# Kernel optimization log

Hardware: AMD Instinct MI355X
Metric: run time of the kernel (lower is better)

The kernel has to match this reference:

```python
import jax, jax.numpy as jnp
import numpy as np
import math

B_, L_, D_, N_ = 8, 2048, 1024, 64


def _ln(x, g, b):
    m = jnp.mean(x, axis=-1, keepdims=True)
    v = jnp.mean((x - m) ** 2, axis=-1, keepdims=True)
    return (x - m) / jnp.sqrt(v + 1e-5) * g + b


def _ssm_kernel(A, Bp, Cp, Dp, L):
    # diagonal SSM: lambda = exp(diag(A)); k[l] = C diag(lambda)^l B + D  -> shape (L,)
    a = jnp.diagonal(A)                                   # (N,)
    powers = jnp.exp(jnp.arange(L)[:, None] * a[None, :])  # (L, N) = lambda^l
    return powers @ (Bp[:, 0] * Cp[0]) + Dp[0]             # (L,)


def _causal_conv(h, k):
    # y[:, t, :] = sum_{j<=t} k[j] * h[:, t-j, :]  via zero-padded FFT (same math, O(L log L))
    L = h.shape[1]
    n = 2 * L
    Hf = jnp.fft.rfft(h, n=n, axis=1)
    Kf = jnp.fft.rfft(k, n=n)
    return jnp.fft.irfft(Hf * Kf[None, :, None], n=n, axis=1)[:, :L]


def _timestep_embedding(t, dim):
    half = dim // 2
    freqs = jnp.exp(jnp.arange(half) * (-math.log(10000.0) / (half - 1)))
    ang = t[:, None] * freqs[None, :]
    return jnp.concatenate([jnp.sin(ang), jnp.cos(ang)], axis=1)  # (B, dim)


def _conv1d(x, w, b):
    # x: (B, C, L), w: (O, I, 3) torch layout, padding=1
    y = jax.lax.conv_general_dilated(x, w, (1,), [(1, 1)],
                                     dimension_numbers=('NCH', 'OIH', 'NCH'))
    return y + b[None, :, None]


def setup_inputs():
    key = jax.random.key(0)
    ks = jax.random.split(key, 26)
    d = {}
    d['x'] = jax.random.normal(ks[0], (B_, L_, D_), jnp.float32)
    d['t'] = jax.random.uniform(ks[1], (B_,), jnp.float32) * 1000.0
    d['beta1'] = jax.random.uniform(ks[2], (1,), jnp.float32)
    d['beta2'] = jax.random.uniform(ks[3], (1,), jnp.float32)
    sc = 1.0 / math.sqrt(D_)
    d['Wi'] = jax.random.normal(ks[4], (D_, D_), jnp.float32) * sc
    d['bi'] = jnp.zeros((D_,), jnp.float32)
    d['Wo'] = jax.random.normal(ks[5], (D_, D_), jnp.float32) * sc
    d['bo'] = jnp.zeros((D_,), jnp.float32)
    d['w1'] = jax.random.normal(ks[6], (D_, D_, 3), jnp.float32) * 0.02
    d['bc1'] = jnp.zeros((D_,), jnp.float32)
    d['w2'] = jax.random.normal(ks[7], (D_, D_, 3), jnp.float32) * 0.02
    d['bc2'] = jnp.zeros((D_,), jnp.float32)
    d['g1'] = jnp.ones((D_,), jnp.float32)
    d['b1'] = jnp.zeros((D_,), jnp.float32)
    d['g2'] = jnp.ones((D_,), jnp.float32)
    d['b2'] = jnp.zeros((D_,), jnp.float32)
    # SSM params (std 0.001 on A keeps exp(l*a) bounded for l up to L)
    d['Af'] = jax.random.normal(ks[8], (N_, N_), jnp.float32) * 0.001
    d['Bf'] = jax.random.normal(ks[9], (N_, 1), jnp.float32) * 0.01
    d['Cf'] = jax.random.normal(ks[10], (1, N_), jnp.float32) * 0.01
    d['Df'] = jax.random.normal(ks[11], (1,), jnp.float32) * 0.01
    d['Ab'] = jax.random.normal(ks[12], (N_, N_), jnp.float32) * 0.001
    d['Bb'] = jax.random.normal(ks[13], (N_, 1), jnp.float32) * 0.01
    d['Cb'] = jax.random.normal(ks[14], (1, N_), jnp.float32) * 0.01
    d['Db'] = jax.random.normal(ks[15], (1,), jnp.float32) * 0.01
    return d


def reference(x, t, beta1, beta2, Wi, bi, Wo, bo, w1, bc1, w2, bc2,
              g1, b1, g2, b2, Af, Bf, Cf, Df, Ab, Bb, Cb, Db):
    Bsz, L, D = x.shape
    h = x @ Wi + bi
    h = _ln(h, g1, b1)
    # local conv branch
    hT = jnp.transpose(h, (0, 2, 1))                 # (B, D, L)
    co = jax.nn.silu(_conv1d(hT, w1, bc1))
    co = _conv1d(co, w2, bc2)
    conv_out = jnp.transpose(co, (0, 2, 1))          # (B, L, D)
    # bidirectional SSM global convolutions
    kf = _ssm_kernel(Af, Bf, Cf, Df, L)
    h_fwd = _causal_conv(h, kf)
    kb = _ssm_kernel(Ab, Bb, Cb, Db, L)
    h_bwd = jnp.flip(_causal_conv(jnp.flip(h, axis=1), kb), axis=1)
    # timestep-conditioned mixing
    noise_scale = jax.nn.sigmoid(_timestep_embedding(t, D))[:, None, :]  # (B,1,D)
    h = h_fwd * (beta1[0] * noise_scale) + h_bwd * (beta2[0] * noise_scale) + conv_out
    h = h @ Wo + bo
    h = _ln(h, g2, b2)
    return x + h
```

## Files before the change

kernel.cpp:

```cpp
#include <hip/hip_runtime.h>

#define Bq 8
#define Lq 2048
#define Dq 1024
#define LPq 2050

typedef unsigned short u16;
typedef __attribute__((ext_vector_type(8))) short bf16x8;
typedef __attribute__((ext_vector_type(4))) float f32x4;

__device__ __forceinline__ u16 f2bf(float f) {
  unsigned u = __float_as_uint(f);
  u += 0x7FFFu + ((u >> 16) & 1u);
  return (u16)(u >> 16);
}
__device__ __forceinline__ float bf2f(u16 s) {
  return __uint_as_float(((unsigned)s) << 16);
}
__device__ __forceinline__ void gld16(const u16* g, u16* l) {
  __builtin_amdgcn_global_load_lds((const __attribute__((address_space(1))) void*)g,
                                   (__attribute__((address_space(3))) void*)l, 16, 0, 0);
}


__global__ __launch_bounds__(256) void prep_small(
    const float* __restrict__ t, const float* __restrict__ beta1, const float* __restrict__ beta2,
    const float* __restrict__ Af, const float* __restrict__ Bf, const float* __restrict__ Cf, const float* __restrict__ Df,
    const float* __restrict__ Ab, const float* __restrict__ Bb, const float* __restrict__ Cb, const float* __restrict__ Db,
    float* __restrict__ kf, float* __restrict__ kb,
    float* __restrict__ c1, float* __restrict__ c2,
    u16* __restrict__ hpad, u16* __restrict__ copad) {
  int tid = blockIdx.x * 256 + threadIdx.x;
  if (blockIdx.x < 8) {
    int l = tid;
    float sf = Df[0], sb = Db[0];
    for (int n = 0; n < 64; n++) {
      sf += __expf((float)l * Af[n * 64 + n]) * (Bf[n] * Cf[n]);
      sb += __expf((float)l * Ab[n * 64 + n]) * (Bb[n] * Cb[n]);
    }
    kf[l] = sf; kb[l] = sb;
  } else if (blockIdx.x < 40) {
    int i = tid - 2048;
    int b = i >> 10, d = i & 1023;
    float tb = t[b];
    float e;
    if (d < 512) {
      float f = __expf((float)d * (-logf(10000.f) / 511.f));
      e = sinf(tb * f);
    } else {
      float f = __expf((float)(d - 512) * (-logf(10000.f) / 511.f));
      e = cosf(tb * f);
    }
    float ns = 1.f / (1.f + __expf(-e));
    c1[i] = beta1[0] * ns;
    c2[i] = beta2[0] * ns;
  } else {
    int i = tid - 10240;
    if (i < 32768) {
      int d = i & 1023;
      int j = i >> 10;
      int arr = j & 1, r = (j >> 1) & 1, b = j >> 2;
      size_t off = (size_t)b * LPq * Dq + (r ? (size_t)(LPq - 1) * Dq : 0) + d;
      if (arr == 0) hpad[off] = 0;
      else          copad[off] = 0;
    }
  }
}

__global__ __launch_bounds__(256) void cast_x(const float* __restrict__ x, u16* __restrict__ xb) {
  size_t i = ((size_t)blockIdx.x * 256 + threadIdx.x) * 8;
  float4 a = *(const float4*)(x + i);
  float4 b = *(const float4*)(x + i + 4);
  u16 o[8] = {f2bf(a.x), f2bf(a.y), f2bf(a.z), f2bf(a.w),
              f2bf(b.x), f2bf(b.y), f2bf(b.z), f2bf(b.w)};
  *(bf16x8*)(xb + i) = *(const bf16x8*)o;
}

__global__ __launch_bounds__(256) void trans_w(const float* __restrict__ W, u16* __restrict__ Wt) {
  __shared__ float tile[64][65];
  int bx = blockIdx.x & 15, by = blockIdx.x >> 4;
  int tx = threadIdx.x & 63, tw = threadIdx.x >> 6;
  for (int r = tw; r < 64; r += 4)
    tile[r][tx] = W[(size_t)(by * 64 + r) * 1024 + bx * 64 + tx];
  __syncthreads();
  for (int r = tw; r < 64; r += 4)
    Wt[(size_t)(bx * 64 + r) * 1024 + by * 64 + tx] = f2bf(tile[tx][r]);
}

__global__ __launch_bounds__(256) void trans_w3(const float* __restrict__ w, u16* __restrict__ Wt) {
  int idx = blockIdx.x * 256 + threadIdx.x;
  int o = idx / 3072, rem = idx % 3072;
  int dt = rem >> 10, i = rem & 1023;
  Wt[idx] = f2bf(w[(size_t)o * 3072 + i * 3 + dt]);
}

__global__ __launch_bounds__(256) void tf_fill(const float* __restrict__ kf, const float* __restrict__ kb,
                                               u16* __restrict__ Tf, u16* __restrict__ Tb) {
  int idx = blockIdx.x * 256 + threadIdx.x;
  int tr = idx >> 9, j0 = (idx & 511) * 4;
  ushort4 vf, vb;
  int j;
  j = j0 + 0; vf.x = (tr >= j) ? f2bf(kf[tr - j]) : (u16)0; vb.x = (j >= tr) ? f2bf(kb[j - tr]) : (u16)0;
  j = j0 + 1; vf.y = (tr >= j) ? f2bf(kf[tr - j]) : (u16)0; vb.y = (j >= tr) ? f2bf(kb[j - tr]) : (u16)0;
  j = j0 + 2; vf.z = (tr >= j) ? f2bf(kf[tr - j]) : (u16)0; vb.z = (j >= tr) ? f2bf(kb[j - tr]) : (u16)0;
  j = j0 + 3; vf.w = (tr >= j) ? f2bf(kf[tr - j]) : (u16)0; vb.w = (j >= tr) ? f2bf(kb[j - tr]) : (u16)0;
  *(ushort4*)(Tf + (size_t)tr * 2048 + j0) = vf;
  *(ushort4*)(Tb + (size_t)tr * 2048 + j0) = vb;
}

__global__ __launch_bounds__(256) void trans_h(const u16* __restrict__ hpad, u16* __restrict__ ht) {
  __shared__ u16 tile[64][66];
  int b = blockIdx.z;
  int lt = blockIdx.x * 64, dt = blockIdx.y * 64;
  int tx = threadIdx.x & 15, ty = threadIdx.x >> 4;
  const u16* src = hpad + (size_t)b * LPq * Dq + (size_t)(lt + 1 + ty) * Dq + dt + tx * 4;
#pragma unroll
  for (int i = 0; i < 4; i++) {
    int r = ty + i * 16;
    ushort4 v = *(const ushort4*)(src + (size_t)i * 16 * Dq);
    tile[tx * 4 + 0][r] = v.x;
    tile[tx * 4 + 1][r] = v.y;
    tile[tx * 4 + 2][r] = v.z;
    tile[tx * 4 + 3][r] = v.w;
  }
  __syncthreads();
#pragma unroll
  for (int i = 0; i < 4; i++) {
    int d = ty + i * 16;
    ushort4 v;
    v.x = tile[d][tx * 4 + 0];
    v.y = tile[d][tx * 4 + 1];
    v.z = tile[d][tx * 4 + 2];
    v.w = tile[d][tx * 4 + 3];
    *(ushort4*)(ht + ((size_t)b * Dq + dt + d) * Lq + lt + tx * 4) = v;
  }
}


__global__ __launch_bounds__(256) void ln1_k(const u16* __restrict__ h0, u16* __restrict__ hpad,
                                             const float* __restrict__ g, const float* __restrict__ be) {
  int w = threadIdx.x >> 6, lane = threadIdx.x & 63;
  int r = blockIdx.x * 4 + w;
  int d0 = lane * 16;
  const u16* hp = h0 + (size_t)r * 1024 + d0;
  bf16x8 va = *(const bf16x8*)hp;
  bf16x8 vb = *(const bf16x8*)(hp + 8);
  float v[16];
#pragma unroll
  for (int i = 0; i < 8; i++) { v[i] = bf2f((u16)va[i]); v[8 + i] = bf2f((u16)vb[i]); }
  float s = 0.f, q = 0.f;
#pragma unroll
  for (int i = 0; i < 16; i++) { s += v[i]; q += v[i] * v[i]; }
#pragma unroll
  for (int o = 32; o > 0; o >>= 1) { s += __shfl_xor(s, o); q += __shfl_xor(q, o); }
  float mean = s * (1.f / 1024.f);
  float rstd = rsqrtf(q * (1.f / 1024.f) - mean * mean + 1e-5f);
  const float4* g4 = (const float4*)(g + d0);
  const float4* b4 = (const float4*)(be + d0);
  u16 o16[16];
#pragma unroll
  for (int i = 0; i < 4; i++) {
    float4 gv = g4[i], bv = b4[i];
    o16[i * 4 + 0] = f2bf((v[i * 4 + 0] - mean) * rstd * gv.x + bv.x);
    o16[i * 4 + 1] = f2bf((v[i * 4 + 1] - mean) * rstd * gv.y + bv.y);
    o16[i * 4 + 2] = f2bf((v[i * 4 + 2] - mean) * rstd * gv.z + bv.z);
    o16[i * 4 + 3] = f2bf((v[i * 4 + 3] - mean) * rstd * gv.w + bv.w);
  }
  int b_ = r >> 11, l = r & 2047;
  u16* dst = hpad + ((size_t)b_ * LPq + l + 1) * Dq + d0;
  *(bf16x8*)dst = *(const bf16x8*)o16;
  *(bf16x8*)(dst + 8) = *(const bf16x8*)(o16 + 8);
}

__global__ __launch_bounds__(256) void ln2_k(const u16* __restrict__ hp, const float* __restrict__ x,
                                             const float* __restrict__ g, const float* __restrict__ be,
                                             float* __restrict__ out) {
  int w = threadIdx.x >> 6, lane = threadIdx.x & 63;
  size_t r = (size_t)blockIdx.x * 4 + w;
  int d0 = lane * 16;
  size_t base = r * 1024 + d0;
  const u16* h = hp + base;
  bf16x8 va = *(const bf16x8*)h;
  bf16x8 vb = *(const bf16x8*)(h + 8);
  float v[16];
#pragma unroll
  for (int i = 0; i < 8; i++) { v[i] = bf2f((u16)va[i]); v[8 + i] = bf2f((u16)vb[i]); }
  float s = 0.f, q = 0.f;
#pragma unroll
  for (int i = 0; i < 16; i++) { s += v[i]; q += v[i] * v[i]; }
#pragma unroll
  for (int o = 32; o > 0; o >>= 1) { s += __shfl_xor(s, o); q += __shfl_xor(q, o); }
  float mean = s * (1.f / 1024.f);
  float rstd = rsqrtf(q * (1.f / 1024.f) - mean * mean + 1e-5f);
  const float4* g4 = (const float4*)(g + d0);
  const float4* b4 = (const float4*)(be + d0);
  const float4* x4 = (const float4*)(x + base);
  float4* o4 = (float4*)(out + base);
#pragma unroll
  for (int i = 0; i < 4; i++) {
    float4 gv = g4[i], bv = b4[i], xv = x4[i];
    float4 o;
    o.x = xv.x + (v[i * 4 + 0] - mean) * rstd * gv.x + bv.x;
    o.y = xv.y + (v[i * 4 + 1] - mean) * rstd * gv.y + bv.y;
    o.z = xv.z + (v[i * 4 + 2] - mean) * rstd * gv.z + bv.z;
    o.w = xv.w + (v[i * 4 + 3] - mean) * rstd * gv.w + bv.w;
    o4[i] = o;
  }
}

__device__ __forceinline__ void gemm_core(const u16* __restrict__ Ab, int lda,
                                          const u16* __restrict__ Bb, int ldb,
                                          int ks, int NS, u16* lds,
                                          f32x4 (&acc)[8][4]) {
  const int t = threadIdx.x;
  const int lane = t & 63, w = t >> 6;
  const int g = w >> 2, j = w & 3;
  const int p1 = t >> 3;
  const int c1 = (t & 7) ^ (p1 & 7);
  const int row1 = (p1 << 1) | (c1 >> 2), f1 = c1 & 3;
  const int q2 = t + 512;
  const int p2 = q2 >> 3;
  const int c2 = (q2 & 7) ^ (p2 & 7);
  const int row2 = (p2 << 1) | (c2 >> 2), f2 = c2 & 3;
  const int aoff1 = row1 * lda + f1 * 8;
  const int aoff2 = row2 * lda + f2 * 8;
  const int boff1 = row1 * ldb + f1 * 8;
  const int boff2 = row2 * ldb + f2 * 8;
  u16* wA1 = lds + t * 8;
  u16* wA2 = lds + 4096 + t * 8;
  u16* wB1 = lds + 8192 + t * 8;
  u16* wB2 = lds + 12288 + t * 8;
  const int frow = lane & 15, fkc = lane >> 4;
  const int arow = g * 128 + frow;
  const int pa = arow >> 1, ca = ((arow & 1) << 2) | fkc;
  const int abase = pa * 64 + ((ca ^ (pa & 7)) << 3);
  const int brow = j * 64 + frow;
  const int pb = brow >> 1, cb = ((brow & 1) << 2) | fkc;
  const int bbase = 8192 + pb * 64 + ((cb ^ (pb & 7)) << 3);

#define STAGE_A(s_) { int sl_ = ((s_) & 3) * 16384; const u16* g_ = Ab + ks + (s_) * 32; \
    gld16(g_ + aoff1, wA1 + sl_); gld16(g_ + aoff2, wA2 + sl_); }
#define STAGE_B(s_) { int sl_ = ((s_) & 3) * 16384; const u16* g_ = Bb + ks + (s_) * 32; \
    gld16(g_ + boff1, wB1 + sl_); gld16(g_ + boff2, wB2 + sl_); }

  STAGE_A(0); STAGE_B(0);
  STAGE_A(1); STAGE_B(1);
  STAGE_A(2); STAGE_B(2);

  for (int s = 0; s < NS; s++) {
    const u16* sl = lds + (s & 3) * 16384;
    if (s <= NS - 3)      { asm volatile("s_waitcnt vmcnt(8)" ::: "memory"); }
    else if (s == NS - 2) { asm volatile("s_waitcnt vmcnt(4)" ::: "memory"); }
    else                  { asm volatile("s_waitcnt vmcnt(0)" ::: "memory"); }
    asm volatile("s_barrier" ::: "memory");
    if (s + 3 < NS) STAGE_A(s + 3);
    bf16x8 bq[4], af[4];
#pragma unroll
    for (int nf = 0; nf < 4; nf++) bq[nf] = *(const bf16x8*)(sl + bbase + nf * 512);
#pragma unroll
    for (int mf = 0; mf < 4; mf++) af[mf] = *(const bf16x8*)(sl + abase + mf * 512);
    __builtin_amdgcn_s_setprio(1);
#pragma unroll
    for (int mf = 0; mf < 4; mf++)
#pragma unroll
      for (int nf = 0; nf < 4; nf++)
        acc[mf][nf] = __builtin_amdgcn_mfma_f32_16x16x32_bf16(af[mf], bq[nf], acc[mf][nf], 0, 0, 0);
    __builtin_amdgcn_s_setprio(0);
    if (s + 3 < NS) STAGE_B(s + 3);
#pragma unroll
    for (int mf = 0; mf < 4; mf++) af[mf] = *(const bf16x8*)(sl + abase + 2048 + mf * 512);
    __builtin_amdgcn_s_setprio(1);
#pragma unroll
    for (int mf = 0; mf < 4; mf++)
#pragma unroll
      for (int nf = 0; nf < 4; nf++)
        acc[4 + mf][nf] = __builtin_amdgcn_mfma_f32_16x16x32_bf16(af[mf], bq[nf], acc[4 + mf][nf], 0, 0, 0);
    __builtin_amdgcn_s_setprio(0);
  }
#undef STAGE_A
#undef STAGE_B
}

template <int MODE>
__global__ __launch_bounds__(512, 2) void gemm8(
    const u16* __restrict__ A, int lda, long abstr,
    const u16* __restrict__ Bw, int ldb,
    u16* __restrict__ Out, long obstr,
    const u16* __restrict__ aux,
    const float* __restrict__ bias, int K, int nbm) {
  __shared__ __align__(16) u16 lds[65536];
  int mb = blockIdx.x % nbm, nb = blockIdx.x / nbm;
  int m0 = mb * 256, n0 = nb * 256;
  int batch = m0 >> 11, r0 = m0 & 2047;
  const u16* Ab = A + (size_t)batch * abstr + (size_t)r0 * lda;
  const u16* Bb = Bw + (size_t)n0 * ldb;
  f32x4 acc[8][4] = {};
  gemm_core(Ab, lda, Bb, ldb, 0, K >> 5, lds, acc);
  int lane = threadIdx.x & 63, w = threadIdx.x >> 6;
  int g = w >> 2, j = w & 3;
  int frow = lane & 15;
  u16* ob = Out + (size_t)batch * obstr;
  const u16* ab2 = (MODE == 3) ? aux + (size_t)batch * obstr : nullptr;
#pragma unroll
  for (int mf = 0; mf < 8; mf++) {
    int row = r0 + g * 128 + mf * 16 + ((lane >> 4) << 2);
#pragma unroll
    for (int nf = 0; nf < 4; nf++) {
      int col = n0 + j * 64 + nf * 16 + frow;
      float bv = bias[col];
      size_t base = (size_t)row * 1024 + col;
      f32x4 a = acc[mf][nf];
#pragma unroll
      for (int i = 0; i < 4; i++) {
        float v = a[i] + bv;
        if (MODE == 1) v = v / (1.f + __expf(-v));
        if (MODE == 3) v += bf2f(ob[base + (size_t)i * 1024]) + bf2f(ab2[base + (size_t)i * 1024]);
        ob[base + (size_t)i * 1024] = f2bf(v);
      }
    }
  }
}

__global__ __launch_bounds__(512, 2) void ssm8(
    const u16* __restrict__ Tf, const u16* __restrict__ Tb,
    const u16* __restrict__ Ht,
    const float* __restrict__ c1, const float* __restrict__ c2,
    u16* __restrict__ outF, u16* __restrict__ outB) {
  __shared__ __align__(16) u16 lds[65536];
  int id = blockIdx.x;
  int dir = id >> 8, r = id & 255;
  int mb = r & 7, nb = r >> 3;
  int m0 = mb * 256, n0 = nb * 256;
  int ks = dir ? m0 : 0;
  int ke = dir ? 2048 : m0 + 256;
  const u16* Tm = dir ? Tb : Tf;
  const u16* Ab = Tm + (size_t)m0 * 2048;
  const u16* Bb = Ht + (size_t)n0 * 2048;
  f32x4 acc[8][4] = {};
  gemm_core(Ab, 2048, Bb, 2048, ks, (ke - ks) >> 5, lds, acc);
  const float* cs = dir ? c2 : c1;
  u16* out = dir ? outB : outF;
  int lane = threadIdx.x & 63, w = threadIdx.x >> 6;
  int g = w >> 2, j = w & 3;
  int frow = lane & 15;
#pragma unroll
  for (int mf = 0; mf < 8; mf++) {
    int row = m0 + g * 128 + mf * 16 + ((lane >> 4) << 2);
#pragma unroll
    for (int nf = 0; nf < 4; nf++) {
      int col = n0 + j * 64 + nf * 16 + frow;
      int b = col >> 10, d = col & 1023;
      float cv = cs[col];
      u16* op = out + ((size_t)b * Lq + row) * 1024 + d;
      f32x4 a = acc[mf][nf];
#pragma unroll
      for (int i = 0; i < 4; i++)
        op[(size_t)i * 1024] = f2bf(a[i] * cv);
    }
  }
}


extern "C" void kernel_launch(void* const* d_in, const int* in_sizes, int n_in,
                              void* d_out, int out_size, void* d_ws, size_t ws_size,
                              hipStream_t stream) {
  const float* x   = (const float*)d_in[0];
  const float* tt  = (const float*)d_in[1];
  const float* be1 = (const float*)d_in[2];
  const float* be2 = (const float*)d_in[3];
  const float* Wi  = (const float*)d_in[4];
  const float* bi  = (const float*)d_in[5];
  const float* Wo  = (const float*)d_in[6];
  const float* bo  = (const float*)d_in[7];
  const float* w1  = (const float*)d_in[8];
  const float* bc1 = (const float*)d_in[9];
  const float* w2  = (const float*)d_in[10];
  const float* bc2 = (const float*)d_in[11];
  const float* g1  = (const float*)d_in[12];
  const float* b1  = (const float*)d_in[13];
  const float* g2  = (const float*)d_in[14];
  const float* b2  = (const float*)d_in[15];
  const float* Af  = (const float*)d_in[16];
  const float* Bf  = (const float*)d_in[17];
  const float* Cf  = (const float*)d_in[18];
  const float* Df  = (const float*)d_in[19];
  const float* Ab  = (const float*)d_in[20];
  const float* Bb  = (const float*)d_in[21];
  const float* Cb  = (const float*)d_in[22];
  const float* Db  = (const float*)d_in[23];

  char* p = (char*)d_ws;
  constexpr size_t SZ_h0   = (size_t)16384 * 1024 * 2;
  constexpr size_t SZ_hpad = (size_t)Bq * LPq * Dq * 2;
  constexpr size_t SZ_ht   = (size_t)Bq * Dq * Lq * 2;
  constexpr size_t SZ_hmix = (size_t)16384 * 1024 * 2;
  constexpr size_t SZ_T    = (size_t)2048 * 2048 * 2;
  constexpr size_t SZ_wt   = (size_t)1024 * 1024 * 2;
  constexpr size_t SZ_w3t  = (size_t)1024 * 3072 * 2;

  size_t off = 0;
  u16* h0    = (u16*)(p + off); off += SZ_h0;
  u16* hpad  = (u16*)(p + off); off += SZ_hpad;
  u16* ht    = (u16*)(p + off); off += SZ_ht;
  u16* copad = (u16*)(p + off); off += SZ_hpad;
  u16* hmixF = (u16*)(p + off); off += SZ_hmix;
  u16* Tf    = (u16*)(p + off); off += SZ_T;
  u16* Tb    = (u16*)(p + off); off += SZ_T;
  u16* wit   = (u16*)(p + off); off += SZ_wt;
  u16* wot   = (u16*)(p + off); off += SZ_wt;
  u16* w1t   = (u16*)(p + off); off += SZ_w3t;
  u16* w2t   = (u16*)(p + off); off += SZ_w3t;
  float* kf  = (float*)(p + off); off += 8192;
  float* kb  = (float*)(p + off); off += 8192;
  float* c1  = (float*)(p + off); off += 32768;
  float* c2  = (float*)(p + off); off += 32768;
  u16* xb    = hmixF;
  u16* hmixB = h0;

  const long BSTR = (long)2048 * 1024;
  const long PSTR = (long)LPq * 1024;

  prep_small<<<dim3(168), dim3(256), 0, stream>>>(tt, be1, be2, Af, Bf, Cf, Df,
                                                  Ab, Bb, Cb, Db, kf, kb, c1, c2, hpad, copad);
  cast_x<<<dim3(8192), dim3(256), 0, stream>>>(x, xb);
  trans_w<<<dim3(256), dim3(256), 0, stream>>>(Wi, wit);
  trans_w<<<dim3(256), dim3(256), 0, stream>>>(Wo, wot);
  trans_w3<<<dim3(12288), dim3(256), 0, stream>>>(w1, w1t);
  trans_w3<<<dim3(12288), dim3(256), 0, stream>>>(w2, w2t);
  tf_fill<<<dim3(4096), dim3(256), 0, stream>>>(kf, kb, Tf, Tb);

  gemm8<0><<<dim3(256), dim3(512), 0, stream>>>(xb, 1024, BSTR, wit, 1024, h0, BSTR, nullptr, bi, 1024, 64);
  ln1_k<<<dim3(4096), dim3(256), 0, stream>>>(h0, hpad, g1, b1);
  trans_h<<<dim3(32, 16, 8), dim3(256), 0, stream>>>(hpad, ht);
  gemm8<1><<<dim3(256), dim3(512), 0, stream>>>(hpad, 1024, PSTR, w1t, 3072, copad + 1024, PSTR, nullptr, bc1, 3072, 64);
  ssm8<<<dim3(512), dim3(512), 0, stream>>>(Tf, Tb, ht, c1, c2, hmixF, hmixB);
  gemm8<3><<<dim3(256), dim3(512), 0, stream>>>(copad, 1024, PSTR, w2t, 3072, hmixF, BSTR, hmixB, bc2, 3072, 64);
  gemm8<0><<<dim3(256), dim3(512), 0, stream>>>(hmixF, 1024, BSTR, wot, 1024, h0, BSTR, nullptr, bo, 1024, 64);
  ln2_k<<<dim3(4096), dim3(256), 0, stream>>>(h0, x, g2, b2, (float*)d_out);
}
```

Measured before the change: 492.6 us.

## Merge prep kernels and co-schedule conv1 GEMM with SSM GEMMs in one launch

Folds the six weight, input and Toeplitz preparation kernels into a single block-indexed launch, and vectorises the w3 transpose to four elements per thread. The first conv GEMM and the two triangular SSM Toeplitz GEMMs now run as one 768-block launch. The forward-direction SSM tiles are reordered so the longest K ranges start first, which should improve load balance against the conv tiles. This cuts launch overhead and fills the GPU with independent work, but the merged kernels share one register and LDS budget and use a fixed branching layout.

```diff
diff --git a/kernel.cpp b/kernel.cpp
--- a/kernel.cpp
+++ b/kernel.cpp
@@ -67,45 +67,60 @@
   }
 }
 
-__global__ __launch_bounds__(256) void cast_x(const float* __restrict__ x, u16* __restrict__ xb) {
-  size_t i = ((size_t)blockIdx.x * 256 + threadIdx.x) * 8;
-  float4 a = *(const float4*)(x + i);
-  float4 b = *(const float4*)(x + i + 4);
-  u16 o[8] = {f2bf(a.x), f2bf(a.y), f2bf(a.z), f2bf(a.w),
-              f2bf(b.x), f2bf(b.y), f2bf(b.z), f2bf(b.w)};
-  *(bf16x8*)(xb + i) = *(const bf16x8*)o;
-}
-
-__global__ __launch_bounds__(256) void trans_w(const float* __restrict__ W, u16* __restrict__ Wt) {
-  __shared__ float tile[64][65];
-  int bx = blockIdx.x & 15, by = blockIdx.x >> 4;
-  int tx = threadIdx.x & 63, tw = threadIdx.x >> 6;
-  for (int r = tw; r < 64; r += 4)
-    tile[r][tx] = W[(size_t)(by * 64 + r) * 1024 + bx * 64 + tx];
-  __syncthreads();
-  for (int r = tw; r < 64; r += 4)
-    Wt[(size_t)(bx * 64 + r) * 1024 + by * 64 + tx] = f2bf(tile[tx][r]);
-}
-
-__global__ __launch_bounds__(256) void trans_w3(const float* __restrict__ w, u16* __restrict__ Wt) {
-  int idx = blockIdx.x * 256 + threadIdx.x;
-  int o = idx / 3072, rem = idx % 3072;
-  int dt = rem >> 10, i = rem & 1023;
-  Wt[idx] = f2bf(w[(size_t)o * 3072 + i * 3 + dt]);
-}
-
-__global__ __launch_bounds__(256) void tf_fill(const float* __restrict__ kf, const float* __restrict__ kb,
-                                               u16* __restrict__ Tf, u16* __restrict__ Tb) {
-  int idx = blockIdx.x * 256 + threadIdx.x;
-  int tr = idx >> 9, j0 = (idx & 511) * 4;
-  ushort4 vf, vb;
-  int j;
-  j = j0 + 0; vf.x = (tr >= j) ? f2bf(kf[tr - j]) : (u16)0; vb.x = (j >= tr) ? f2bf(kb[j - tr]) : (u16)0;
-  j = j0 + 1; vf.y = (tr >= j) ? f2bf(kf[tr - j]) : (u16)0; vb.y = (j >= tr) ? f2bf(kb[j - tr]) : (u16)0;
-  j = j0 + 2; vf.z = (tr >= j) ? f2bf(kf[tr - j]) : (u16)0; vb.z = (j >= tr) ? f2bf(kb[j - tr]) : (u16)0;
-  j = j0 + 3; vf.w = (tr >= j) ? f2bf(kf[tr - j]) : (u16)0; vb.w = (j >= tr) ? f2bf(kb[j - tr]) : (u16)0;
-  *(ushort4*)(Tf + (size_t)tr * 2048 + j0) = vf;
-  *(ushort4*)(Tb + (size_t)tr * 2048 + j0) = vb;
+__global__ __launch_bounds__(256) void mega_prep(
+    const float* __restrict__ x, u16* __restrict__ xb,
+    const float* __restrict__ Wi, u16* __restrict__ wit,
+    const float* __restrict__ Wo, u16* __restrict__ wot,
+    const float* __restrict__ w1, u16* __restrict__ w1t,
+    const float* __restrict__ w2, u16* __restrict__ w2t,
+    const float* __restrict__ kf, const float* __restrict__ kb,
+    u16* __restrict__ Tf, u16* __restrict__ Tb) {
+  int bid = blockIdx.x, tid = threadIdx.x;
+  if (bid < 8192) {
+    size_t i = ((size_t)bid * 256 + tid) * 8;
+    float4 a = *(const float4*)(x + i);
+    float4 b = *(const float4*)(x + i + 4);
+    u16 o[8] = {f2bf(a.x), f2bf(a.y), f2bf(a.z), f2bf(a.w),
+                f2bf(b.x), f2bf(b.y), f2bf(b.z), f2bf(b.w)};
+    *(bf16x8*)(xb + i) = *(const bf16x8*)o;
+  } else if (bid < 8704) {
+    __shared__ float tile[64][65];
+    const float* W = (bid < 8448) ? Wi : Wo;
+    u16* Wt = (bid < 8448) ? wit : wot;
+    int b2 = (bid < 8448) ? bid - 8192 : bid - 8448;
+    int bx = b2 & 15, by = b2 >> 4;
+    int tx = tid & 63, tw = tid >> 6;
+    for (int r = tw; r < 64; r += 4)
+      tile[r][tx] = W[(size_t)(by * 64 + r) * 1024 + bx * 64 + tx];
+    __syncthreads();
+    for (int r = tw; r < 64; r += 4)
+      Wt[(size_t)(bx * 64 + r) * 1024 + by * 64 + tx] = f2bf(tile[tx][r]);
+  } else if (bid < 14848) {
+    const float* w = (bid < 11776) ? w1 : w2;
+    u16* Wt = (bid < 11776) ? w1t : w2t;
+    int vb = (bid < 11776) ? bid - 8704 : bid - 11776;
+    int base = (vb * 256 + tid) * 4;
+    int o = base / 3072, rem = base % 3072;
+    int dt = rem >> 10, i0 = rem & 1023;
+    const float* src = w + (size_t)o * 3072 + dt;
+    ushort4 v;
+    v.x = f2bf(src[(i0 + 0) * 3]);
+    v.y = f2bf(src[(i0 + 1) * 3]);
+    v.z = f2bf(src[(i0 + 2) * 3]);
+    v.w = f2bf(src[(i0 + 3) * 3]);
+    *(ushort4*)(Wt + base) = v;
+  } else {
+    int idx = (bid - 14848) * 256 + tid;
+    int tr = idx >> 9, j0 = (idx & 511) * 4;
+    ushort4 vf, vb4;
+    int j;
+    j = j0 + 0; vf.x = (tr >= j) ? f2bf(kf[tr - j]) : (u16)0; vb4.x = (j >= tr) ? f2bf(kb[j - tr]) : (u16)0;
+    j = j0 + 1; vf.y = (tr >= j) ? f2bf(kf[tr - j]) : (u16)0; vb4.y = (j >= tr) ? f2bf(kb[j - tr]) : (u16)0;
+    j = j0 + 2; vf.z = (tr >= j) ? f2bf(kf[tr - j]) : (u16)0; vb4.z = (j >= tr) ? f2bf(kb[j - tr]) : (u16)0;
+    j = j0 + 3; vf.w = (tr >= j) ? f2bf(kf[tr - j]) : (u16)0; vb4.w = (j >= tr) ? f2bf(kb[j - tr]) : (u16)0;
+    *(ushort4*)(Tf + (size_t)tr * 2048 + j0) = vf;
+    *(ushort4*)(Tb + (size_t)tr * 2048 + j0) = vb4;
+  }
 }
 
 __global__ __launch_bounds__(256) void trans_h(const u16* __restrict__ hpad, u16* __restrict__ ht) {
@@ -321,41 +336,74 @@
   }
 }
 
-__global__ __launch_bounds__(512, 2) void ssm8(
+__global__ __launch_bounds__(512, 2) void mix8(
+    const u16* __restrict__ hpad, const u16* __restrict__ w1t,
+    u16* __restrict__ co, const float* __restrict__ bc1,
     const u16* __restrict__ Tf, const u16* __restrict__ Tb,
     const u16* __restrict__ Ht,
     const float* __restrict__ c1, const float* __restrict__ c2,
     u16* __restrict__ outF, u16* __restrict__ outB) {
   __shared__ __align__(16) u16 lds[65536];
+  const long PSTR = (long)LPq * 1024;
   int id = blockIdx.x;
-  int dir = id >> 8, r = id & 255;
-  int mb = r & 7, nb = r >> 3;
-  int m0 = mb * 256, n0 = nb * 256;
-  int ks = dir ? m0 : 0;
-  int ke = dir ? 2048 : m0 + 256;
-  const u16* Tm = dir ? Tb : Tf;
-  const u16* Ab = Tm + (size_t)m0 * 2048;
-  const u16* Bb = Ht + (size_t)n0 * 2048;
-  f32x4 acc[8][4] = {};
-  gemm_core(Ab, 2048, Bb, 2048, ks, (ke - ks) >> 5, lds, acc);
-  const float* cs = dir ? c2 : c1;
-  u16* out = dir ? outB : outF;
   int lane = threadIdx.x & 63, w = threadIdx.x >> 6;
   int g = w >> 2, j = w & 3;
   int frow = lane & 15;
-#pragma unroll
-  for (int mf = 0; mf < 8; mf++) {
-    int row = m0 + g * 128 + mf * 16 + ((lane >> 4) << 2);
-#pragma unroll
-    for (int nf = 0; nf < 4; nf++) {
-      int col = n0 + j * 64 + nf * 16 + frow;
-      int b = col >> 10, d = col & 1023;
-      float cv = cs[col];
-      u16* op = out + ((size_t)b * Lq + row) * 1024 + d;
-      f32x4 a = acc[mf][nf];
-#pragma unroll
-      for (int i = 0; i < 4; i++)
-        op[(size_t)i * 1024] = f2bf(a[i] * cv);
+  if (id < 256) {
+    int mb = id & 63, nb = id >> 6;
+    int m0 = mb * 256, n0 = nb * 256;
+    int batch = m0 >> 11, r0 = m0 & 2047;
+    const u16* Ab = hpad + (size_t)batch * PSTR + (size_t)r0 * 1024;
+    const u16* Bb = w1t + (size_t)n0 * 3072;
+    f32x4 acc[8][4] = {};
+    gemm_core(Ab, 1024, Bb, 3072, 0, 96, lds, acc);
+    u16* ob = co + (size_t)batch * PSTR;
+#pragma unroll
+    for (int mf = 0; mf < 8; mf++) {
+      int row = r0 + g * 128 + mf * 16 + ((lane >> 4) << 2);
+#pragma unroll
+      for (int nf = 0; nf < 4; nf++) {
+        int col = n0 + j * 64 + nf * 16 + frow;
+        float bv = bc1[col];
+        size_t base = (size_t)row * 1024 + col;
+        f32x4 a = acc[mf][nf];
+#pragma unroll
+        for (int i = 0; i < 4; i++) {
+          float v = a[i] + bv;
+          v = v / (1.f + __expf(-v));
+          ob[base + (size_t)i * 1024] = f2bf(v);
+        }
+      }
+    }
+  } else {
+    int rr = id - 256;
+    int dir = rr >> 8, r = rr & 255;
+    int mb = dir ? (r & 7) : (7 - (r & 7));
+    int nb = r >> 3;
+    int m0 = mb * 256, n0 = nb * 256;
+    int ks = dir ? m0 : 0;
+    int ke = dir ? 2048 : m0 + 256;
+    const u16* Tm = dir ? Tb : Tf;
+    const u16* Ab = Tm + (size_t)m0 * 2048;
+    const u16* Bb = Ht + (size_t)n0 * 2048;
+    f32x4 acc[8][4] = {};
+    gemm_core(Ab, 2048, Bb, 2048, ks, (ke - ks) >> 5, lds, acc);
+    const float* cs = dir ? c2 : c1;
+    u16* out = dir ? outB : outF;
+#pragma unroll
+    for (int mf = 0; mf < 8; mf++) {
+      int row = m0 + g * 128 + mf * 16 + ((lane >> 4) << 2);
+#pragma unroll
+      for (int nf = 0; nf < 4; nf++) {
+        int col = n0 + j * 64 + nf * 16 + frow;
+        int b = col >> 10, d = col & 1023;
+        float cv = cs[col];
+        u16* op = out + ((size_t)b * Lq + row) * 1024 + d;
+        f32x4 a = acc[mf][nf];
+#pragma unroll
+        for (int i = 0; i < 4; i++)
+          op[(size_t)i * 1024] = f2bf(a[i] * cv);
+      }
     }
   }
 }
@@ -422,18 +470,14 @@
 
   prep_small<<<dim3(168), dim3(256), 0, stream>>>(tt, be1, be2, Af, Bf, Cf, Df,
                                                   Ab, Bb, Cb, Db, kf, kb, c1, c2, hpad, copad);
-  cast_x<<<dim3(8192), dim3(256), 0, stream>>>(x, xb);
-  trans_w<<<dim3(256), dim3(256), 0, stream>>>(Wi, wit);
-  trans_w<<<dim3(256), dim3(256), 0, stream>>>(Wo, wot);
-  trans_w3<<<dim3(12288), dim3(256), 0, stream>>>(w1, w1t);
-  trans_w3<<<dim3(12288), dim3(256), 0, stream>>>(w2, w2t);
-  tf_fill<<<dim3(4096), dim3(256), 0, stream>>>(kf, kb, Tf, Tb);
+  mega_prep<<<dim3(18944), dim3(256), 0, stream>>>(x, xb, Wi, wit, Wo, wot,
+                                                   w1, w1t, w2, w2t, kf, kb, Tf, Tb);
 
   gemm8<0><<<dim3(256), dim3(512), 0, stream>>>(xb, 1024, BSTR, wit, 1024, h0, BSTR, nullptr, bi, 1024, 64);
   ln1_k<<<dim3(4096), dim3(256), 0, stream>>>(h0, hpad, g1, b1);
   trans_h<<<dim3(32, 16, 8), dim3(256), 0, stream>>>(hpad, ht);
-  gemm8<1><<<dim3(256), dim3(512), 0, stream>>>(hpad, 1024, PSTR, w1t, 3072, copad + 1024, PSTR, nullptr, bc1, 3072, 64);
-  ssm8<<<dim3(512), dim3(512), 0, stream>>>(Tf, Tb, ht, c1, c2, hmixF, hmixB);
+  mix8<<<dim3(768), dim3(512), 0, stream>>>(hpad, w1t, copad + 1024, bc1,
+                                            Tf, Tb, ht, c1, c2, hmixF, hmixB);
   gemm8<3><<<dim3(256), dim3(512), 0, stream>>>(copad, 1024, PSTR, w2t, 3072, hmixF, BSTR, hmixB, bc2, 3072, 64);
   gemm8<0><<<dim3(256), dim3(512), 0, stream>>>(hmixF, 1024, BSTR, wot, 1024, h0, BSTR, nullptr, bo, 1024, 64);
   ln2_k<<<dim3(4096), dim3(256), 0, stream>>>(h0, x, g2, b2, (float*)d_out);
```

New measurement: 496.9 us. About the same (+0.9%).
